# Kernel optimization log

Hardware: AMD Instinct MI355X
Metric: run time of the kernel (lower is better)

Reference implementation:

```python
import jax, jax.numpy as jnp
import numpy as np

# LoFTR coarse-matching config (eval path, no padding masks)
THR = 0.2
BORDER_RM = 2
TEMP = 0.1
H0C, W0C = 60, 80  # L = 4800
H1C, W1C = 60, 80  # S = 4800
N, C = 2, 256


def _border_valid(h, w, bd):
    # flat [h*w] bool, False within bd of any border of the (h, w) grid
    hi = jnp.arange(h)
    wi = jnp.arange(w)
    vh = (hi >= bd) & (hi < h - bd)
    vw = (wi >= bd) & (wi < w - bd)
    return (vh[:, None] & vw[None, :]).reshape(-1)


def setup_inputs() -> dict:
    key = jax.random.key(0)
    k0, k1 = jax.random.split(key)
    feat_c0 = jax.random.normal(k0, (N, H0C * W0C, C), dtype=jnp.float32)
    feat_c1 = jax.random.normal(k1, (N, H1C * W1C, C), dtype=jnp.float32)
    return {"feat_c0": feat_c0, "feat_c1": feat_c1}


def reference(feat_c0, feat_c1):
    c = feat_c0.shape[-1]
    inv_sqrt_c = 1.0 / (float(c) ** 0.5)
    f0 = feat_c0 * inv_sqrt_c
    f1 = feat_c1 * inv_sqrt_c
    # [N, L, S] similarity
    sim = jnp.einsum('nlc,nsc->nls', f0, f1) / TEMP
    # dual softmax
    conf = jax.nn.softmax(sim, axis=1) * jax.nn.softmax(sim, axis=2)
    # threshold + border removal
    mask = conf > THR
    valid0 = _border_valid(H0C, W0C, BORDER_RM)  # [L]
    valid1 = _border_valid(H1C, W1C, BORDER_RM)  # [S]
    mask = mask & valid0[None, :, None] & valid1[None, None, :]
    # mutual nearest neighbour
    mask = mask \
        & (conf == jnp.max(conf, axis=2, keepdims=True)) \
        & (conf == jnp.max(conf, axis=1, keepdims=True))
    return conf, mask
```

## Files before the change

kernel.cpp:

```cpp
#include <hip/hip_runtime.h>
#include <hip/hip_bf16.h>
#include <cstdint>

static constexpr int   Nb = 2;
static constexpr int   L  = 4800;
static constexpr int   S  = 4800;
static constexpr int   C  = 256;
static constexpr float THR = 0.2f;
static constexpr float SIM_SCALE = 1.0f / 25.6f;
static constexpr unsigned CAND_CAP = 65536;

using f32x4  = __attribute__((ext_vector_type(4))) float;
using bf16x8 = __attribute__((ext_vector_type(8))) short;
using u32x4  = __attribute__((ext_vector_type(4))) unsigned int;
using u16x4  = __attribute__((ext_vector_type(4))) unsigned short;

__global__ __launch_bounds__(256) void init_stats(unsigned int* __restrict__ p, int n) {
    int i = blockIdx.x * 256 + threadIdx.x;
    if (i < n) p[i] = 0u;
}

__device__ inline unsigned short bf16_rne(float x) {
    unsigned u = __float_as_uint(x);
    unsigned r = (u + 0x7FFFu + ((u >> 16) & 1u)) >> 16;
    return (unsigned short)r;
}

__global__ __launch_bounds__(256) void cvt_bf16(const float* __restrict__ in0,
                                                const float* __restrict__ in1,
                                                unsigned short* __restrict__ out0,
                                                unsigned short* __restrict__ out1,
                                                int n8) {
    const float* in = blockIdx.y ? in1 : in0;
    unsigned short* out = blockIdx.y ? out1 : out0;
    int i = blockIdx.x * 256 + threadIdx.x;
    if (i >= n8) return;
    f32x4 a = *(const f32x4*)(in + (size_t)i * 8);
    f32x4 b = *(const f32x4*)(in + (size_t)i * 8 + 4);
    union { unsigned short us[8]; u32x4 v; } r;
#pragma unroll
    for (int j = 0; j < 4; j++) r.us[j] = bf16_rne(a[j]);
#pragma unroll
    for (int j = 0; j < 4; j++) r.us[4 + j] = bf16_rne(b[j]);
    *(u32x4*)(out + (size_t)i * 8) = r.v;
}

__device__ inline bool border_ok(int idx) {
    int h = idx / 80, w = idx % 80;
    return (h >= 2) & (h < 58) & (w >= 2) & (w < 78);
}

#define BM 96
#define BK 64

__device__ inline void gload16(const void* g, void* l) {
    __builtin_amdgcn_global_load_lds(
        (const __attribute__((address_space(1))) unsigned int*)g,
        (__attribute__((address_space(3))) unsigned int*)l, 16, 0, 0);
}

__global__ __launch_bounds__(256) void gemm_sums_e(
    const unsigned short* __restrict__ Abf,
    const unsigned short* __restrict__ Bbf,
    unsigned short* __restrict__ eh,
    float* __restrict__ rowSum,
    float* __restrict__ colSum,
    float* __restrict__ mask)
{
    __shared__ unsigned short As[BM * BK];
    __shared__ unsigned short Bs[BM * BK];

    const int n  = blockIdx.z;
    const int rb = blockIdx.y * BM;
    const int cb = blockIdx.x * BM;
    const int t  = threadIdx.x;
    const int lane = t & 63;
    const int wid  = t >> 6;
    const int wr = wid >> 1, wc = wid & 1;

    const unsigned short* Ag = Abf + ((size_t)n * L + rb) * C;
    const unsigned short* Bg = Bbf + ((size_t)n * S + cb) * C;

    f32x4 acc[3][3] = {};

    for (int kt = 0; kt < C; kt += BK) {
#pragma unroll
        for (int i = 0; i < 3; i++) {
            int idx = wid * 192 + i * 64 + lane;
            int row = idx >> 3;
            int src = ((idx & 7) ^ (row & 7)) * 8 + kt;
            void* ldsA = &As[(wid * 192 + i * 64) * 8];
            void* ldsB = &Bs[(wid * 192 + i * 64) * 8];
            gload16(Ag + (size_t)row * C + src, ldsA);
            gload16(Bg + (size_t)row * C + src, ldsB);
        }
        __syncthreads();

#pragma unroll
        for (int kk = 0; kk < 2; kk++) {
            bf16x8 a[3], b[3];
            const int kElem = kk * 32 + (lane >> 4) * 8;
#pragma unroll
            for (int f = 0; f < 3; f++) {
                int ra = wr * 48 + f * 16 + (lane & 15);
                a[f] = *(const bf16x8*)&As[ra * 64 + (kElem ^ ((ra & 7) << 3))];
                int rbi = wc * 48 + f * 16 + (lane & 15);
                b[f] = *(const bf16x8*)&Bs[rbi * 64 + (kElem ^ ((rbi & 7) << 3))];
            }
#pragma unroll
            for (int fi = 0; fi < 3; fi++)
#pragma unroll
                for (int fj = 0; fj < 3; fj++)
                    acc[fi][fj] = __builtin_amdgcn_mfma_f32_16x16x32_bf16(
                        b[fj], a[fi], acc[fi][fj], 0, 0, 0);
        }
        __syncthreads();
    }

    const int rowBase = rb + wr * 48;
    const int colBase = cb + wc * 48;
    float csum[3][4] = {};

#pragma unroll
    for (int fi = 0; fi < 3; fi++) {
        const int l = rowBase + fi * 16 + (lane & 15);
        float rsum = 0.f;
#pragma unroll
        for (int fj = 0; fj < 3; fj++) {
            const int s0 = colBase + fj * 16 + ((lane >> 4) << 2);
            union { _Float16 h[4]; u16x4 v; } pk;
#pragma unroll
            for (int r = 0; r < 4; r++) {
                float e = __expf(acc[fi][fj][r] * SIM_SCALE);
                rsum += e;
                csum[fj][r] += e;
                pk.h[r] = (_Float16)e;
            }
            *(u16x4*)&eh[((size_t)n * L + l) * S + s0] = pk.v;
        }
        rsum += __shfl_xor(rsum, 16);
        rsum += __shfl_xor(rsum, 32);
        if (lane < 16)
            atomicAdd(&rowSum[(size_t)n * L + l], rsum);
    }
#pragma unroll
    for (int fj = 0; fj < 3; fj++)
#pragma unroll
        for (int r = 0; r < 4; r++) {
            float v = csum[fj][r];
            v += __shfl_xor(v, 1);
            v += __shfl_xor(v, 2);
            v += __shfl_xor(v, 4);
            v += __shfl_xor(v, 8);
            if ((lane & 15) == 0)
                atomicAdd(&colSum[(size_t)n * S + colBase + fj * 16 + ((lane >> 4) << 2) + r], v);
        }

    const f32x4 zero4 = {0.f, 0.f, 0.f, 0.f};
    const size_t bid = ((size_t)blockIdx.z * gridDim.y + blockIdx.y) * gridDim.x + blockIdx.x;
    const size_t mbase = bid * 9216;
#pragma unroll
    for (int i = 0; i < 9; i++)
        *(f32x4*)&mask[mbase + ((size_t)i * 256 + t) * 4] = zero4;
}

__global__ __launch_bounds__(256) void stream_conf(
    const unsigned short* __restrict__ eh,
    const float* __restrict__ rowSum,
    const float* __restrict__ colSum,
    float* __restrict__ conf,
    unsigned* __restrict__ rowMax,
    unsigned* __restrict__ colMax,
    unsigned* __restrict__ cnt,
    unsigned* __restrict__ cand)
{
    const int ROWS = 32;
    const int CBLK = 19;
    const int tilesPerN = (L / ROWS) * CBLK;
    const int wid = threadIdx.x >> 6, lane = threadIdx.x & 63;
    const int tw = blockIdx.x * 4 + wid;
    if (tw >= Nb * tilesPerN) return;
    const int n   = tw / tilesPerN;
    const int rem = tw % tilesPerN;
    const int r0  = (rem / CBLK) * ROWS;
    const int c   = (rem % CBLK) * 256 + lane * 4;
    const bool act = (c < S);

    f32x4 invD1 = {0.f, 0.f, 0.f, 0.f};
    bool bs[4] = {false, false, false, false};
    if (act) {
        f32x4 d1 = *(const f32x4*)&colSum[(size_t)n * S + c];
#pragma unroll
        for (int j = 0; j < 4; j++) { invD1[j] = 1.0f / d1[j]; bs[j] = border_ok(c + j); }
    }
    f32x4 cmax = {0.f, 0.f, 0.f, 0.f};

    for (int r = r0; r < r0 + ROWS; r++) {
        const float invD2 = 1.0f / rowSum[(size_t)n * L + r];
        const bool bl = border_ok(r);
        float rmax = 0.f;
        if (act) {
            union { u16x4 v; _Float16 h[4]; } ev;
            ev.v = *(const u16x4*)&eh[((size_t)n * L + r) * S + c];
            f32x4 cv;
#pragma unroll
            for (int j = 0; j < 4; j++) {
                float e = (float)ev.h[j];
                float cf = e * e * invD1[j] * invD2;
                cv[j] = cf;
                rmax = fmaxf(rmax, cf);
                cmax[j] = fmaxf(cmax[j], cf);
                if (cf > THR && bl && bs[j]) {
                    unsigned pos = atomicAdd(cnt, 1u);
                    if (pos < CAND_CAP) {
                        unsigned flat = (unsigned)(((size_t)n * L + r) * S + c + j);
                        cand[2 * pos]     = flat;
                        cand[2 * pos + 1] = __float_as_uint(cf);
                    }
                }
            }
            *(f32x4*)&conf[((size_t)n * L + r) * S + c] = cv;
        }
#pragma unroll
        for (int d = 1; d < 64; d <<= 1) rmax = fmaxf(rmax, __shfl_xor(rmax, d));
        if (lane == 0)
            atomicMax(&rowMax[(size_t)n * L + r], __float_as_uint(rmax));
    }
    if (act) {
#pragma unroll
        for (int j = 0; j < 4; j++)
            atomicMax(&colMax[(size_t)n * S + c + j], __float_as_uint(cmax[j]));
    }
}

__global__ __launch_bounds__(256) void mask_scatter(
    const unsigned* __restrict__ cnt,
    const unsigned* __restrict__ cand,
    const unsigned* __restrict__ rowMax,
    const unsigned* __restrict__ colMax,
    float* __restrict__ mask)
{
    unsigned nc = *cnt;
    if (nc > CAND_CAP) nc = CAND_CAP;
    for (unsigned i = blockIdx.x * 256 + threadIdx.x; i < nc; i += gridDim.x * 256) {
        unsigned flat = cand[2 * i];
        unsigned bits = cand[2 * i + 1];
        unsigned row = flat / S;
        unsigned s   = flat % S;
        unsigned n   = row / L;
        if (bits == rowMax[row] && bits == colMax[n * S + s])
            mask[flat] = 1.0f;
    }
}

extern "C" void kernel_launch(void* const* d_in, const int* in_sizes, int n_in,
                              void* d_out, int out_size, void* d_ws, size_t ws_size,
                              hipStream_t stream) {
    (void)in_sizes; (void)n_in; (void)out_size; (void)ws_size;
    const float* f0 = (const float*)d_in[0];
    const float* f1 = (const float*)d_in[1];

    float* conf = (float*)d_out;
    float* mask = conf + (size_t)Nb * L * S;

    unsigned short* Abf = (unsigned short*)d_ws;
    unsigned short* Bbf = Abf + (size_t)Nb * L * C;
    float* rowSum = (float*)(Bbf + (size_t)Nb * S * C);
    float* colSum = rowSum + (size_t)Nb * L;
    unsigned* rowMax = (unsigned*)(colSum + (size_t)Nb * S);
    unsigned* colMax = rowMax + (size_t)Nb * L;
    unsigned* cnt    = colMax + (size_t)Nb * S;
    unsigned* cand   = cnt + 2;
    unsigned short* eh = (unsigned short*)(cand + 2 * CAND_CAP);

    const int nStats = 2 * (Nb * L + Nb * S) + 1;
    init_stats<<<(nStats + 255) / 256, 256, 0, stream>>>((unsigned*)rowSum, nStats);

    const int n8 = Nb * L * C / 8;
    cvt_bf16<<<dim3((n8 + 255) / 256, 2), 256, 0, stream>>>(f0, f1, Abf, Bbf, n8);

    gemm_sums_e<<<dim3(S / BM, L / BM, Nb), 256, 0, stream>>>(Abf, Bbf, eh, rowSum, colSum, mask);

    const int nTiles = Nb * (L / 32) * 19;
    stream_conf<<<(nTiles + 3) / 4, 256, 0, stream>>>(eh, rowSum, colSum, conf,
                                                      rowMax, colMax, cnt, cand);

    mask_scatter<<<32, 256, 0, stream>>>(cnt, cand, rowMax, colMax, mask);
}
```

Baseline: 172.9 us.

## Widen GEMM tile, stage exp output through LDS, remap blocks per XCD, fuse init

The GEMM tile is widened from 96x96 to 96x192 so each A tile is reused across twice as many columns. The fp16 exp tile is now staged in shared memory with an XOR swizzle and written to global memory as coalesced 16-byte rows instead of scattered 8-byte stores. The launch grid becomes 1D with an XCD-aware remap so neighbouring tiles share L2. Stats zeroing moves into the bf16 convert kernel to drop one launch. In exchange, the larger accumulator array raises register pressure and the extra LDS barrier adds a sync point.

Result: faster. 169.0 us (-2.2%).

```diff
diff --git a/kernel.cpp b/kernel.cpp
--- a/kernel.cpp
+++ b/kernel.cpp
@@ -13,24 +13,22 @@
 using f32x4  = __attribute__((ext_vector_type(4))) float;
 using bf16x8 = __attribute__((ext_vector_type(8))) short;
 using u32x4  = __attribute__((ext_vector_type(4))) unsigned int;
-using u16x4  = __attribute__((ext_vector_type(4))) unsigned short;
-
-__global__ __launch_bounds__(256) void init_stats(unsigned int* __restrict__ p, int n) {
-    int i = blockIdx.x * 256 + threadIdx.x;
-    if (i < n) p[i] = 0u;
-}
 
 __device__ inline unsigned short bf16_rne(float x) {
     unsigned u = __float_as_uint(x);
-    unsigned r = (u + 0x7FFFu + ((u >> 16) & 1u)) >> 16;
-    return (unsigned short)r;
+    return (unsigned short)((u + 0x7FFFu + ((u >> 16) & 1u)) >> 16);
 }
 
 __global__ __launch_bounds__(256) void cvt_bf16(const float* __restrict__ in0,
                                                 const float* __restrict__ in1,
                                                 unsigned short* __restrict__ out0,
                                                 unsigned short* __restrict__ out1,
-                                                int n8) {
+                                                int n8,
+                                                unsigned* __restrict__ stats, int nStats) {
+    if (blockIdx.y == 0) {
+        int si = blockIdx.x * 256 + threadIdx.x;
+        if (si < nStats) stats[si] = 0u;
+    }
     const float* in = blockIdx.y ? in1 : in0;
     unsigned short* out = blockIdx.y ? out1 : out0;
     int i = blockIdx.x * 256 + threadIdx.x;
@@ -51,7 +49,14 @@
 }
 
 #define BM 96
+#define BN 192
 #define BK 64
+
+static constexpr int NWG   = (L / BM) * (S / BN) * Nb;
+static constexpr int TILE_X = S / BN;
+static constexpr int TILES_PER_N = (L / BM) * TILE_X;
+static constexpr int XQ = NWG / 8;
+static constexpr int XR = NWG % 8;
 
 __device__ inline void gload16(const void* g, void* l) {
     __builtin_amdgcn_global_load_lds(
@@ -67,12 +72,19 @@
     float* __restrict__ colSum,
     float* __restrict__ mask)
 {
-    __shared__ unsigned short As[BM * BK];
-    __shared__ unsigned short Bs[BM * BK];
-
-    const int n  = blockIdx.z;
-    const int rb = blockIdx.y * BM;
-    const int cb = blockIdx.x * BM;
+    __shared__ __align__(16) unsigned short smem[BM * BK + BN * BK];
+    unsigned short* As = smem;
+    unsigned short* Bs = smem + BM * BK;
+
+    const int orig = blockIdx.x;
+    const int xcd  = orig & 7;
+    const int idx  = orig >> 3;
+    const int wgid = (xcd < XR ? xcd * (XQ + 1) : XR * (XQ + 1) + (xcd - XR) * XQ) + idx;
+    const int n    = wgid / TILES_PER_N;
+    const int rem  = wgid % TILES_PER_N;
+    const int rb   = (rem / TILE_X) * BM;
+    const int cb   = (rem % TILE_X) * BN;
+
     const int t  = threadIdx.x;
     const int lane = t & 63;
     const int wid  = t >> 6;
@@ -81,54 +93,58 @@
     const unsigned short* Ag = Abf + ((size_t)n * L + rb) * C;
     const unsigned short* Bg = Bbf + ((size_t)n * S + cb) * C;
 
-    f32x4 acc[3][3] = {};
+    f32x4 acc[3][6] = {};
 
     for (int kt = 0; kt < C; kt += BK) {
 #pragma unroll
         for (int i = 0; i < 3; i++) {
-            int idx = wid * 192 + i * 64 + lane;
-            int row = idx >> 3;
-            int src = ((idx & 7) ^ (row & 7)) * 8 + kt;
-            void* ldsA = &As[(wid * 192 + i * 64) * 8];
-            void* ldsB = &Bs[(wid * 192 + i * 64) * 8];
-            gload16(Ag + (size_t)row * C + src, ldsA);
-            gload16(Bg + (size_t)row * C + src, ldsB);
+            int ix = wid * 192 + i * 64 + lane;
+            int row = ix >> 3;
+            int src = ((ix & 7) ^ (row & 7)) * 8 + kt;
+            gload16(Ag + (size_t)row * C + src, &As[(wid * 192 + i * 64) * 8]);
+        }
+#pragma unroll
+        for (int i = 0; i < 6; i++) {
+            int ix = wid * 384 + i * 64 + lane;
+            int row = ix >> 3;
+            int src = ((ix & 7) ^ (row & 7)) * 8 + kt;
+            gload16(Bg + (size_t)row * C + src, &Bs[(wid * 384 + i * 64) * 8]);
         }
         __syncthreads();
 
 #pragma unroll
         for (int kk = 0; kk < 2; kk++) {
-            bf16x8 a[3], b[3];
+            bf16x8 a[3], b[6];
             const int kElem = kk * 32 + (lane >> 4) * 8;
 #pragma unroll
             for (int f = 0; f < 3; f++) {
                 int ra = wr * 48 + f * 16 + (lane & 15);
                 a[f] = *(const bf16x8*)&As[ra * 64 + (kElem ^ ((ra & 7) << 3))];
-                int rbi = wc * 48 + f * 16 + (lane & 15);
+            }
+#pragma unroll
+            for (int f = 0; f < 6; f++) {
+                int rbi = wc * 96 + f * 16 + (lane & 15);
                 b[f] = *(const bf16x8*)&Bs[rbi * 64 + (kElem ^ ((rbi & 7) << 3))];
             }
 #pragma unroll
             for (int fi = 0; fi < 3; fi++)
 #pragma unroll
-                for (int fj = 0; fj < 3; fj++)
+                for (int fj = 0; fj < 6; fj++)
                     acc[fi][fj] = __builtin_amdgcn_mfma_f32_16x16x32_bf16(
                         b[fj], a[fi], acc[fi][fj], 0, 0, 0);
         }
         __syncthreads();
     }
 
-    const int rowBase = rb + wr * 48;
-    const int colBase = cb + wc * 48;
-    float csum[3][4] = {};
-
+    float csum[6][4] = {};
 #pragma unroll
     for (int fi = 0; fi < 3; fi++) {
-        const int l = rowBase + fi * 16 + (lane & 15);
+        const int bl = wr * 48 + fi * 16 + (lane & 15);
         float rsum = 0.f;
 #pragma unroll
-        for (int fj = 0; fj < 3; fj++) {
-            const int s0 = colBase + fj * 16 + ((lane >> 4) << 2);
-            union { _Float16 h[4]; u16x4 v; } pk;
+        for (int fj = 0; fj < 6; fj++) {
+            const int bs = wc * 96 + fj * 16 + ((lane >> 4) << 2);
+            union { _Float16 h[4]; unsigned long long u; } pk;
 #pragma unroll
             for (int r = 0; r < 4; r++) {
                 float e = __expf(acc[fi][fj][r] * SIM_SCALE);
@@ -136,15 +152,16 @@
                 csum[fj][r] += e;
                 pk.h[r] = (_Float16)e;
             }
-            *(u16x4*)&eh[((size_t)n * L + l) * S + s0] = pk.v;
+            unsigned off = bl * 384 + ((bs * 2) ^ ((bl & 7) << 4));
+            *(unsigned long long*)((char*)smem + off) = pk.u;
         }
         rsum += __shfl_xor(rsum, 16);
         rsum += __shfl_xor(rsum, 32);
         if (lane < 16)
-            atomicAdd(&rowSum[(size_t)n * L + l], rsum);
-    }
-#pragma unroll
-    for (int fj = 0; fj < 3; fj++)
+            atomicAdd(&rowSum[(size_t)n * L + rb + bl], rsum);
+    }
+#pragma unroll
+    for (int fj = 0; fj < 6; fj++)
 #pragma unroll
         for (int r = 0; r < 4; r++) {
             float v = csum[fj][r];
@@ -153,14 +170,25 @@
             v += __shfl_xor(v, 4);
             v += __shfl_xor(v, 8);
             if ((lane & 15) == 0)
-                atomicAdd(&colSum[(size_t)n * S + colBase + fj * 16 + ((lane >> 4) << 2) + r], v);
-        }
+                atomicAdd(&colSum[(size_t)n * S + cb + wc * 96 + fj * 16 + ((lane >> 4) << 2) + r], v);
+        }
+    __syncthreads();
+
+    const size_t ebase = ((size_t)n * L + rb) * S + cb;
+#pragma unroll
+    for (int i = 0; i < 9; i++) {
+        int chunk = i * 256 + t;
+        int row = chunk / 24;
+        int k   = chunk % 24;
+        unsigned lb = row * 384 + ((k * 16) ^ ((row & 7) << 4));
+        u32x4 v = *(const u32x4*)((const char*)smem + lb);
+        *(u32x4*)&eh[ebase + (size_t)row * S + k * 8] = v;
+    }
 
     const f32x4 zero4 = {0.f, 0.f, 0.f, 0.f};
-    const size_t bid = ((size_t)blockIdx.z * gridDim.y + blockIdx.y) * gridDim.x + blockIdx.x;
-    const size_t mbase = bid * 9216;
-#pragma unroll
-    for (int i = 0; i < 9; i++)
+    const size_t mbase = (size_t)wgid * 18432;
+#pragma unroll
+    for (int i = 0; i < 18; i++)
         *(f32x4*)&mask[mbase + ((size_t)i * 256 + t) * 4] = zero4;
 }
 
@@ -187,11 +215,11 @@
     const bool act = (c < S);
 
     f32x4 invD1 = {0.f, 0.f, 0.f, 0.f};
-    bool bs[4] = {false, false, false, false};
+    bool bs4[4] = {false, false, false, false};
     if (act) {
         f32x4 d1 = *(const f32x4*)&colSum[(size_t)n * S + c];
 #pragma unroll
-        for (int j = 0; j < 4; j++) { invD1[j] = 1.0f / d1[j]; bs[j] = border_ok(c + j); }
+        for (int j = 0; j < 4; j++) { invD1[j] = 1.0f / d1[j]; bs4[j] = border_ok(c + j); }
     }
     f32x4 cmax = {0.f, 0.f, 0.f, 0.f};
 
@@ -200,8 +228,8 @@
         const bool bl = border_ok(r);
         float rmax = 0.f;
         if (act) {
-            union { u16x4 v; _Float16 h[4]; } ev;
-            ev.v = *(const u16x4*)&eh[((size_t)n * L + r) * S + c];
+            union { unsigned long long u; _Float16 h[4]; } ev;
+            ev.u = *(const unsigned long long*)&eh[((size_t)n * L + r) * S + c];
             f32x4 cv;
 #pragma unroll
             for (int j = 0; j < 4; j++) {
@@ -210,11 +238,10 @@
                 cv[j] = cf;
                 rmax = fmaxf(rmax, cf);
                 cmax[j] = fmaxf(cmax[j], cf);
-                if (cf > THR && bl && bs[j]) {
+                if (cf > THR && bl && bs4[j]) {
                     unsigned pos = atomicAdd(cnt, 1u);
                     if (pos < CAND_CAP) {
-                        unsigned flat = (unsigned)(((size_t)n * L + r) * S + c + j);
-                        cand[2 * pos]     = flat;
+                        cand[2 * pos]     = (unsigned)(((size_t)n * L + r) * S + c + j);
                         cand[2 * pos + 1] = __float_as_uint(cf);
                     }
                 }
@@ -270,16 +297,15 @@
     unsigned* rowMax = (unsigned*)(colSum + (size_t)Nb * S);
     unsigned* colMax = rowMax + (size_t)Nb * L;
     unsigned* cnt    = colMax + (size_t)Nb * S;
-    unsigned* cand   = cnt + 2;
+    unsigned* cand   = cnt + 4;
     unsigned short* eh = (unsigned short*)(cand + 2 * CAND_CAP);
 
-    const int nStats = 2 * (Nb * L + Nb * S) + 1;
-    init_stats<<<(nStats + 255) / 256, 256, 0, stream>>>((unsigned*)rowSum, nStats);
-
+    const int nStats = 2 * (Nb * L + Nb * S) + 4;
     const int n8 = Nb * L * C / 8;
-    cvt_bf16<<<dim3((n8 + 255) / 256, 2), 256, 0, stream>>>(f0, f1, Abf, Bbf, n8);
-
-    gemm_sums_e<<<dim3(S / BM, L / BM, Nb), 256, 0, stream>>>(Abf, Bbf, eh, rowSum, colSum, mask);
+    cvt_bf16<<<dim3((n8 + 255) / 256, 2), 256, 0, stream>>>(f0, f1, Abf, Bbf, n8,
+                                                            (unsigned*)rowSum, nStats);
+
+    gemm_sums_e<<<NWG, 256, 0, stream>>>(Abf, Bbf, eh, rowSum, colSum, mask);
 
     const int nTiles = Nb * (L / 32) * 19;
     stream_conf<<<(nTiles + 3) / 4, 256, 0, stream>>>(eh, rowSum, colSum, conf,
```
